# Optimization experiments

Measured on AMD Instinct MI355X. Metric: run time of the kernel, lower is better.

## Reference

```python
import jax, jax.numpy as jnp
import numpy as np

B, D, H, E, K = 8192, 1024, 4096, 8, 2
LOSS_COEF = 0.01
EPS_COMBINE = float(np.finfo(np.float64).eps)  # np.finfo(float).eps used in combine


def setup_inputs() -> dict:
    key = jax.random.key(0)
    ks = jax.random.split(key, 6)
    s_in = 1.0 / np.sqrt(D)
    s_hid = 1.0 / np.sqrt(H)
    return {
        "x": jax.random.normal(ks[0], (B, D), jnp.float32),
        "w_gate": jax.random.uniform(ks[1], (E, D), jnp.float32, -s_in, s_in),
        "fc1_w": jax.random.uniform(ks[2], (E, H, D), jnp.float32, -s_in, s_in),
        "fc1_b": jax.random.uniform(ks[3], (E, H), jnp.float32, -s_in, s_in),
        "fc2_w": jax.random.uniform(ks[4], (E, D, H), jnp.float32, -s_hid, s_hid),
        "fc2_b": jax.random.uniform(ks[5], (E, D), jnp.float32, -s_hid, s_hid),
    }


def _cv_squared(v):
    # torch .var() uses ddof=1
    return jnp.var(v, ddof=1) / (jnp.mean(v) ** 2 + 1e-10)


def _top_k_gating(x, w_gate):
    # clean logits (noisy_gating=False): [B, E]
    logits = x @ w_gate.T
    top_vals, top_idx = jax.lax.top_k(logits, K + 1)  # min(k+1, E)
    topk_vals = top_vals[:, :K]
    topk_idx = top_idx[:, :K]
    topk_gates = jax.nn.softmax(topk_vals, axis=1)
    gates = jnp.zeros((x.shape[0], E), x.dtype)
    gates = gates.at[jnp.arange(x.shape[0])[:, None], topk_idx].set(topk_gates)
    return gates


def _forward(x, w_gate, fc1_w, fc1_b, fc2_w, fc2_b):
    gates = _top_k_gating(x, w_gate)            # [B, E], sparse (k nonzeros/row)
    importance = gates.sum(axis=0)              # [E]
    load = (gates > 0).sum(axis=0).astype(jnp.float32)
    loss = (_cv_squared(importance) + _cv_squared(load)) * LOSS_COEF

    # Dense-equivalent expert compute: tokens with gate==0 contribute 0 to the
    # combine, identical math to SparseDispatcher's gather/scatter.
    h = jnp.einsum('bd,ehd->beh', x, fc1_w) + fc1_b            # [B, E, H]
    h = jax.nn.gelu(h, approximate=False)                      # torch exact gelu
    o = jnp.einsum('beh,edh->bed', h, fc2_w) + fc2_b           # [B, E, D]
    log_p = jax.nn.log_softmax(o, axis=-1)                     # LogSoftmax(dim=1)

    # combine: exp, weight by gates, scatter-add, eps-fill, log
    combined = jnp.einsum('be,bed->bd', gates, jnp.exp(log_p)) # [B, D]
    combined = jnp.where(combined == 0, EPS_COMBINE, combined)
    y = jnp.log(combined)
    return y, loss


def reference(x, w_gate, fc1_w, fc1_b, fc2_w, fc2_b):
    return _forward(x, w_gate, fc1_w, fc1_b, fc2_w, fc2_b)
```

## Files before the change

### kernel.cpp

```cpp
#include <hip/hip_runtime.h>
#include <cstdint>
#include <cmath>

#define BT 8192
#define DD 1024
#define HH 4096
#define EE 8
#define MT2 72

typedef __attribute__((ext_vector_type(8))) short short8;
typedef __attribute__((ext_vector_type(4))) float f32x4;
typedef unsigned short u16;
typedef unsigned int u32;

__device__ __forceinline__ u16 f2bf(float f) {
    u32 u = __float_as_uint(f);
    u += 0x7FFFu + ((u >> 16) & 1u);
    return (u16)(u >> 16);
}

__device__ __forceinline__ void gld_lds16(const void* g, void* l) {
    __builtin_amdgcn_global_load_lds((__attribute__((address_space(1))) void*)g,
                                     (__attribute__((address_space(3))) void*)l,
                                     16, 0, 0);
}

__global__ void cvt_kernel(const float* __restrict__ src, u16* __restrict__ dst, int n8) {
    int i = blockIdx.x * blockDim.x + threadIdx.x;
    if (i >= n8) return;
    size_t base = (size_t)i * 8;
    float4 a = *(const float4*)(src + base);
    float4 b = *(const float4*)(src + base + 4);
    uint4 o;
    o.x = (u32)f2bf(a.x) | ((u32)f2bf(a.y) << 16);
    o.y = (u32)f2bf(a.z) | ((u32)f2bf(a.w) << 16);
    o.z = (u32)f2bf(b.x) | ((u32)f2bf(b.y) << 16);
    o.w = (u32)f2bf(b.z) | ((u32)f2bf(b.w) << 16);
    *(uint4*)(dst + base) = o;
}

__global__ void gating_kernel(const float* __restrict__ x, const float* __restrict__ wg,
                              float* __restrict__ gate_arr, int* __restrict__ list,
                              int* __restrict__ info,
                              int* __restrict__ counts, float* __restrict__ importance) {
    int wave = (blockIdx.x * blockDim.x + threadIdx.x) >> 6;
    int lane = threadIdx.x & 63;
    if (wave >= BT) return;
    const float* xr = x + (size_t)wave * DD;
    double acc[EE];
#pragma unroll
    for (int e = 0; e < EE; ++e) acc[e] = 0.0;
#pragma unroll
    for (int c = 0; c < DD / 256; ++c) {
        const int i = c * 256 + lane * 4;
        float4 xv = *(const float4*)(xr + i);
        double x0 = xv.x, x1 = xv.y, x2 = xv.z, x3 = xv.w;
#pragma unroll
        for (int e = 0; e < EE; ++e) {
            float4 wv = *(const float4*)(wg + e * DD + i);
            acc[e] += x0 * (double)wv.x + x1 * (double)wv.y
                    + x2 * (double)wv.z + x3 * (double)wv.w;
        }
    }
#pragma unroll
    for (int e = 0; e < EE; ++e) {
        double v = acc[e];
        for (int off = 32; off; off >>= 1) v += __shfl_down(v, off, 64);
        acc[e] = v;
    }
    if (lane == 0) {
        int i0 = 0; double v0 = acc[0];
        for (int e = 1; e < EE; ++e) if (acc[e] > v0) { v0 = acc[e]; i0 = e; }
        int i1 = -1; double v1 = -1e300;
        for (int e = 0; e < EE; ++e) { if (e == i0) continue; if (acc[e] > v1) { v1 = acc[e]; i1 = e; } }
        double e1 = exp(v1 - v0);
        double s = 1.0 + e1;
        float g0 = (float)(1.0 / s);
        float g1 = (float)(e1 / s);
        gate_arr[2 * wave]     = g0;
        gate_arr[2 * wave + 1] = g1;
        atomicAdd(&importance[i0], g0);
        atomicAdd(&importance[i1], g1);
        int p0 = atomicAdd(&counts[i0], 1);
        list[i0 * BT + p0] = wave;
        int p1 = atomicAdd(&counts[i1], 1);
        list[i1 * BT + p1] = wave;
        info[2 * wave]     = (i0 << 16) | p0;
        info[2 * wave + 1] = (i1 << 16) | p1;
    }
}

__global__ void loss_kernel(const int* __restrict__ counts, const float* __restrict__ importance,
                            int* __restrict__ offs, float* __restrict__ out_loss,
                            int* __restrict__ tmap, int* __restrict__ ntiles) {
    if (threadIdx.x == 0 && blockIdx.x == 0) {
        double mi = 0, ml = 0;
        int off = 0;
        for (int e = 0; e < EE; e++) {
            offs[e] = off; off += counts[e];
            mi += (double)importance[e]; ml += (double)counts[e];
        }
        mi /= EE; ml /= EE;
        double vi = 0, vl = 0;
        for (int e = 0; e < EE; e++) {
            double di = (double)importance[e] - mi; vi += di * di;
            double dl = (double)counts[e] - ml;     vl += dl * dl;
        }
        vi /= (EE - 1); vl /= (EE - 1);
        double cv_i = vi / (mi * mi + 1e-10);
        double cv_l = vl / (ml * ml + 1e-10);
        *out_loss = (float)((cv_i + cv_l) * 0.01);
        int ntl = 0;
        for (int e = 0; e < EE; e++)
            for (int t = 0; t < counts[e]; t += 256)
                tmap[ntl++] = (e << 20) | t;
        *ntiles = ntl;
    }
}

__global__ void gather_x_kernel(const float* __restrict__ x, const int* __restrict__ list,
                                const int* __restrict__ counts, const int* __restrict__ offs,
                                u16* __restrict__ xg) {
    int r = blockIdx.x;
    int e = 0;
#pragma unroll
    for (int i = 1; i < EE; ++i) if (r >= offs[i]) e = i;
    int m = r - offs[e];
    if (m >= counts[e]) return;
    int token = list[e * BT + m];
    const float* src = x + (size_t)token * DD;
    u16* dst = xg + (size_t)r * DD;
    int i = threadIdx.x * 4;
    float4 a = *(const float4*)(src + i);
    uint2 o;
    o.x = (u32)f2bf(a.x) | ((u32)f2bf(a.y) << 16);
    o.y = (u32)f2bf(a.z) | ((u32)f2bf(a.w) << 16);
    *(uint2*)(dst + i) = o;
}

template <int K, int NT, bool GELU, bool GATHER>
__global__ __launch_bounds__(512) void moe_gemm(const u16* __restrict__ Asrc,
                                                const u16* __restrict__ Bsrc,
                                                const float* __restrict__ bias,
                                                const int* __restrict__ list,
                                                const int* __restrict__ counts,
                                                const int* __restrict__ offs,
                                                const int* __restrict__ tmap,
                                                const int* __restrict__ ntiles,
                                                u16* __restrict__ outB,
                                                float* __restrict__ outF) {
    constexpr int NXT = NT / 256;
    constexpr int nwg = NXT * MT2;
    constexpr int QW = nwg / 8;
    constexpr int ITERS = K / 128;
    const int tid = threadIdx.x;
    const int lane = tid & 63;
    const int wv = tid >> 6;
    const int wqr = wv >> 2;
    const int wqc = wv & 3;
    const int kq = lane >> 4;
    const int rsub = lane & 15;
    const int rq = kq * 4;
    const int ks1 = tid >> 7;
    const int r128 = tid & 127;

    __shared__ u16 Ls[2][2][2][8192];

    const int nw = *ntiles;

#define STAGE_A(db, h, T)                                                   \
    do {                                                                    \
        gld_lds16(aP##h + (T) * 64,      &Ls[db][0][h][tid * 8]);           \
        gld_lds16(aP##h + (T) * 64 + 32, &Ls[db][0][h][(tid + 512) * 8]);   \
    } while (0)
#define STAGE_B(db, h, T)                                                   \
    do {                                                                    \
        gld_lds16(bP##h + (T) * 64,      &Ls[db][1][h][tid * 8]);           \
        gld_lds16(bP##h + (T) * 64 + 32, &Ls[db][1][h][(tid + 512) * 8]);   \
    } while (0)
#define WAIT4 asm volatile("s_waitcnt vmcnt(4)" ::: "memory")
#define WAIT0 asm volatile("s_waitcnt vmcnt(0)" ::: "memory")
#define BAR __builtin_amdgcn_s_barrier()

#define READ_A(db, mh)                                                        \
    do {                                                                      \
        _Pragma("unroll") for (int kk = 0; kk < 2; kk++)                      \
        _Pragma("unroll") for (int mi = 0; mi < 4; mi++)                      \
            afr[mi][kk] = *(const short8*)&Ls[db][0][mh]                      \
                [((kk * 4 + kq) * 128 + wqr * 64 + mi * 16 + rsub) * 8];      \
    } while (0)
#define READ_B(nh, db)                                                        \
    do {                                                                      \
        _Pragma("unroll") for (int kk = 0; kk < 2; kk++)                      \
        _Pragma("unroll") for (int ni = 0; ni < 2; ni++)                      \
            bfr[nh][ni][kk] = *(const short8*)&Ls[db][1][nh]                  \
                [((kk * 4 + kq) * 128 + wqc * 32 + ni * 16 + rsub) * 8];      \
    } while (0)
#define MFMAQ(mh, nh)                                                         \
    do {                                                                      \
        __builtin_amdgcn_s_setprio(1);                                        \
        _Pragma("unroll") for (int mi = 0; mi < 4; mi++)                      \
        _Pragma("unroll") for (int ni = 0; ni < 2; ni++)                      \
        _Pragma("unroll") for (int kk = 0; kk < 2; kk++)                      \
            acc[mh][nh][mi][ni] = __builtin_amdgcn_mfma_f32_16x16x32_bf16(    \
                afr[mi][kk], bfr[nh][ni][kk], acc[mh][nh][mi][ni], 0, 0, 0);  \
        __builtin_amdgcn_s_setprio(0);                                        \
    } while (0)

#pragma unroll 1
    for (int raw = blockIdx.x; raw < nwg; raw += 256) {
        const int wg = (raw & 7) * QW + (raw >> 3);
        const int nt = wg / MT2;
        const int mt = wg - nt * MT2;
        if (mt >= nw) continue;
        const int ent = tmap[mt];
        const int e = ent >> 20;
        const int mbase = ent & 0xFFFFF;
        const int mmax = counts[e] - mbase;
        const int rowbase = offs[e] + mbase;
        const int nbase = nt * 256;

        size_t arow0, arow1;
        if constexpr (GATHER) {
            arow0 = (size_t)list[e * BT + mbase + min(r128, mmax - 1)];
            arow1 = (size_t)list[e * BT + mbase + min(128 + r128, mmax - 1)];
        } else {
            arow0 = (size_t)(rowbase + min(r128, mmax - 1));
            arow1 = (size_t)(rowbase + min(128 + r128, mmax - 1));
        }
        const u16* aP0 = Asrc + arow0 * (size_t)K + ks1 * 8;
        const u16* aP1 = Asrc + arow1 * (size_t)K + ks1 * 8;
        const u16* bP0 = Bsrc + ((size_t)e * NT + nbase + r128) * (size_t)K + ks1 * 8;
        const u16* bP1 = bP0 + (size_t)128 * K;

        f32x4 acc[2][2][4][2] = {};
        short8 afr[4][2];
        short8 bfr[2][2][2];

        STAGE_A(0, 0, 0); STAGE_B(0, 0, 0); STAGE_A(0, 1, 0); STAGE_B(0, 1, 0);
        STAGE_A(1, 0, 1); STAGE_B(1, 0, 1);
        WAIT4;
        BAR;

#pragma unroll 1
        for (int it = 0; it < ITERS - 1; ++it) {
            const int t = 2 * it;
            READ_A(0, 0); READ_B(0, 0); STAGE_A(1, 1, t + 1); MFMAQ(0, 0); BAR;
            READ_B(1, 0); STAGE_B(1, 1, t + 1); MFMAQ(0, 1); BAR;
            READ_A(0, 1); STAGE_A(0, 0, t + 2); MFMAQ(1, 0); BAR;
            STAGE_B(0, 0, t + 2); MFMAQ(1, 1); WAIT4; BAR;
            READ_A(1, 0); READ_B(0, 1); STAGE_A(0, 1, t + 2); MFMAQ(0, 0); BAR;
            READ_B(1, 1); STAGE_B(0, 1, t + 2); MFMAQ(0, 1); BAR;
            READ_A(1, 1); STAGE_A(1, 0, t + 3); MFMAQ(1, 0); BAR;
            STAGE_B(1, 0, t + 3); MFMAQ(1, 1); WAIT4; BAR;
        }
        {
            const int t = 2 * (ITERS - 1);
            READ_A(0, 0); READ_B(0, 0); STAGE_A(1, 1, t + 1); MFMAQ(0, 0); BAR;
            READ_B(1, 0); STAGE_B(1, 1, t + 1); MFMAQ(0, 1); BAR;
            READ_A(0, 1); MFMAQ(1, 0); BAR;
            MFMAQ(1, 1); WAIT0; BAR;
            READ_A(1, 0); READ_B(0, 1); MFMAQ(0, 0); BAR;
            READ_B(1, 1); MFMAQ(0, 1); BAR;
            READ_A(1, 1); MFMAQ(1, 0); BAR;
            MFMAQ(1, 1); BAR;
        }

        float bvals[2][2];
#pragma unroll
        for (int nh = 0; nh < 2; nh++)
#pragma unroll
            for (int ni = 0; ni < 2; ni++)
                bvals[nh][ni] = bias[(size_t)e * NT + nbase + nh * 128 + wqc * 32 + ni * 16 + rsub];
#pragma unroll
        for (int mh = 0; mh < 2; mh++) {
#pragma unroll
            for (int mi = 0; mi < 4; mi++) {
#pragma unroll
                for (int r = 0; r < 4; r++) {
                    int m = mh * 128 + wqr * 64 + mi * 16 + rq + r;
                    if (m < mmax) {
                        size_t ro = (size_t)(rowbase + m);
#pragma unroll
                        for (int nh = 0; nh < 2; nh++) {
#pragma unroll
                            for (int ni = 0; ni < 2; ni++) {
                                int n = nbase + nh * 128 + wqc * 32 + ni * 16 + rsub;
                                float v = acc[mh][nh][mi][ni][r] + bvals[nh][ni];
                                if constexpr (GELU) {
                                    v = 0.5f * v * (1.0f + erff(v * 0.7071067811865476f));
                                    outB[ro * NT + n] = f2bf(v);
                                } else {
                                    outF[ro * NT + n] = v;
                                }
                            }
                        }
                    }
                }
            }
        }
        WAIT0;
    }
#undef READ_A
#undef READ_B
#undef MFMAQ
#undef STAGE_A
#undef STAGE_B
#undef WAIT4
#undef WAIT0
#undef BAR
}

__global__ void combine_kernel(const float* __restrict__ o, const float* __restrict__ gates,
                               const int* __restrict__ info, const int* __restrict__ offs,
                               float* __restrict__ y) {
    const int b = blockIdx.x;
    const int tid = threadIdx.x;
    const int lane = tid & 63, wv = tid >> 6;
    const int inf0 = info[2 * b], inf1 = info[2 * b + 1];
    const int r0i = offs[inf0 >> 16] + (inf0 & 0xffff);
    const int r1i = offs[inf1 >> 16] + (inf1 & 0xffff);
    const float* r0 = o + (size_t)r0i * DD;
    const float* r1 = o + (size_t)r1i * DD;
    float v0[4], v1[4];
#pragma unroll
    for (int j = 0; j < 4; j++) { v0[j] = r0[tid + 256 * j]; v1[j] = r1[tid + 256 * j]; }
    float m0 = fmaxf(fmaxf(v0[0], v0[1]), fmaxf(v0[2], v0[3]));
    float m1 = fmaxf(fmaxf(v1[0], v1[1]), fmaxf(v1[2], v1[3]));
#pragma unroll
    for (int off = 32; off; off >>= 1) {
        m0 = fmaxf(m0, __shfl_xor(m0, off, 64));
        m1 = fmaxf(m1, __shfl_xor(m1, off, 64));
    }
    __shared__ float sred[2][4];
    if (lane == 0) { sred[0][wv] = m0; sred[1][wv] = m1; }
    __syncthreads();
    m0 = fmaxf(fmaxf(sred[0][0], sred[0][1]), fmaxf(sred[0][2], sred[0][3]));
    m1 = fmaxf(fmaxf(sred[1][0], sred[1][1]), fmaxf(sred[1][2], sred[1][3]));
    float p0[4], p1[4], s0 = 0.f, s1 = 0.f;
#pragma unroll
    for (int j = 0; j < 4; j++) {
        p0[j] = expf(v0[j] - m0); s0 += p0[j];
        p1[j] = expf(v1[j] - m1); s1 += p1[j];
    }
#pragma unroll
    for (int off = 32; off; off >>= 1) {
        s0 += __shfl_xor(s0, off, 64);
        s1 += __shfl_xor(s1, off, 64);
    }
    __shared__ float sred2[2][4];
    if (lane == 0) { sred2[0][wv] = s0; sred2[1][wv] = s1; }
    __syncthreads();
    s0 = sred2[0][0] + sred2[0][1] + sred2[0][2] + sred2[0][3];
    s1 = sred2[1][0] + sred2[1][1] + sred2[1][2] + sred2[1][3];
    const float c0 = gates[2 * b] / s0;
    const float c1 = gates[2 * b + 1] / s1;
#pragma unroll
    for (int j = 0; j < 4; j++) {
        float c = p0[j] * c0 + p1[j] * c1;
        if (c == 0.f) c = 2.2204460492503131e-16f;
        y[(size_t)b * DD + tid + 256 * j] = logf(c);
    }
}

extern "C" void kernel_launch(void* const* d_in, const int* in_sizes, int n_in,
                              void* d_out, int out_size, void* d_ws, size_t ws_size,
                              hipStream_t stream) {
    const float* x     = (const float*)d_in[0];
    const float* wgate = (const float*)d_in[1];
    const float* fc1w  = (const float*)d_in[2];
    const float* fc1b  = (const float*)d_in[3];
    const float* fc2w  = (const float*)d_in[4];
    const float* fc2b  = (const float*)d_in[5];
    float* out = (float*)d_out;

    char* ws = (char*)d_ws;
    const size_t MB = 1024 * 1024;
    const bool big = ws_size >= 289 * MB;
    u16* w1b = (u16*)(ws);
    float* o = (float*)(ws);
    u16* w2b = (u16*)(ws + 64 * MB);
    u16* xb  = (u16*)(ws + 128 * MB);
    u16* h   = (u16*)(ws + (big ? 128 : 144) * MB);
    u16* xg  = (u16*)(ws + 256 * MB);
    char* meta = ws + (big ? 288 : 272) * MB;
    int* counts       = (int*)meta;
    int* offs         = (int*)(meta + 32);
    float* importance = (float*)(meta + 64);
    int* ntiles       = (int*)(meta + 96);
    float* gate_arr   = (float*)(meta + 128);
    int* info         = (int*)(meta + 128 + 65536);
    int* list         = (int*)(meta + 128 + 131072);
    int* tmap         = (int*)(meta + 512 * 1024);

    hipMemsetAsync(meta, 0, 96, stream);
    cvt_kernel<<<(EE * HH * DD / 8 + 255) / 256, 256, 0, stream>>>(fc1w, w1b, EE * HH * DD / 8);
    cvt_kernel<<<(EE * DD * HH / 8 + 255) / 256, 256, 0, stream>>>(fc2w, w2b, EE * DD * HH / 8);
    gating_kernel<<<BT / 4, 256, 0, stream>>>(x, wgate, gate_arr, list, info, counts, importance);
    loss_kernel<<<1, 64, 0, stream>>>(counts, importance, offs, out + (size_t)BT * DD, tmap, ntiles);

    if (big) {
        gather_x_kernel<<<2 * BT, 256, 0, stream>>>(x, list, counts, offs, xg);
        moe_gemm<DD, HH, true, false><<<256, 512, 0, stream>>>(
            xg, w1b, fc1b, nullptr, counts, offs, tmap, ntiles, h, nullptr);
    } else {
        cvt_kernel<<<(BT * DD / 8 + 255) / 256, 256, 0, stream>>>(x, xb, BT * DD / 8);
        moe_gemm<DD, HH, true, true><<<256, 512, 0, stream>>>(
            xb, w1b, fc1b, list, counts, offs, tmap, ntiles, h, nullptr);
    }
    moe_gemm<HH, DD, false, false><<<256, 512, 0, stream>>>(
        h, w2b, fc2b, nullptr, counts, offs, tmap, ntiles, nullptr, o);
    combine_kernel<<<BT, 256, 0, stream>>>(o, gate_arr, info, offs, out);
}
```

Baseline: 1.174 ms.

## Shrink MoE GEMM output tile to 256x128 with a single B buffer

Changes the expert GEMM workgroup tile from 256x256 to 256x128 (M x N). The 8 waves are rearranged as 4x2, each computing 64x64 instead of 128x64. LDS staging now holds two A halves and one B buffer per stage, and the pipeline is restructured into four MFMA phases per iteration with adjusted vmcnt waits. This doubles the number of N tiles, which gives more workgroups for the persistent loop and cuts LDS use. The cost is lower arithmetic intensity: A is re-read twice as often from global memory, and there is more barrier overhead per MFMA.

```diff
diff --git a/kernel.cpp b/kernel.cpp
--- a/kernel.cpp
+++ b/kernel.cpp
@@ -149,57 +149,59 @@
                                                 const int* __restrict__ ntiles,
                                                 u16* __restrict__ outB,
                                                 float* __restrict__ outF) {
-    constexpr int NXT = NT / 256;
+    constexpr int NXT = NT / 128;
     constexpr int nwg = NXT * MT2;
     constexpr int QW = nwg / 8;
     constexpr int ITERS = K / 128;
     const int tid = threadIdx.x;
     const int lane = tid & 63;
     const int wv = tid >> 6;
-    const int wqr = wv >> 2;
-    const int wqc = wv & 3;
+    const int wqm = wv >> 1;
+    const int wqn = wv & 1;
     const int kq = lane >> 4;
     const int rsub = lane & 15;
     const int rq = kq * 4;
     const int ks1 = tid >> 7;
     const int r128 = tid & 127;
 
-    __shared__ u16 Ls[2][2][2][8192];
+    __shared__ u16 Ls[2][3][8192];
 
     const int nw = *ntiles;
 
 #define STAGE_A(db, h, T)                                                   \
     do {                                                                    \
-        gld_lds16(aP##h + (T) * 64,      &Ls[db][0][h][tid * 8]);           \
-        gld_lds16(aP##h + (T) * 64 + 32, &Ls[db][0][h][(tid + 512) * 8]);   \
+        gld_lds16(aP##h + (T) * 64,      &Ls[db][h][tid * 8]);              \
+        gld_lds16(aP##h + (T) * 64 + 32, &Ls[db][h][(tid + 512) * 8]);      \
     } while (0)
-#define STAGE_B(db, h, T)                                                   \
+#define STAGE_B(db, T)                                                      \
     do {                                                                    \
-        gld_lds16(bP##h + (T) * 64,      &Ls[db][1][h][tid * 8]);           \
-        gld_lds16(bP##h + (T) * 64 + 32, &Ls[db][1][h][(tid + 512) * 8]);   \
+        gld_lds16(bP + (T) * 64,      &Ls[db][2][tid * 8]);                 \
+        gld_lds16(bP + (T) * 64 + 32, &Ls[db][2][(tid + 512) * 8]);         \
     } while (0)
-#define WAIT4 asm volatile("s_waitcnt vmcnt(4)" ::: "memory")
+#define WAIT2 asm volatile("s_waitcnt vmcnt(2)" ::: "memory")
 #define WAIT0 asm volatile("s_waitcnt vmcnt(0)" ::: "memory")
 #define BAR __builtin_amdgcn_s_barrier()
 
 #define READ_A(db, mh)                                                        \
     do {                                                                      \
         _Pragma("unroll") for (int kk = 0; kk < 2; kk++)                      \
-        _Pragma("unroll") for (int mi = 0; mi < 4; mi++)                      \
-            afr[mi][kk] = *(const short8*)&Ls[db][0][mh]                      \
-                [((kk * 4 + kq) * 128 + wqr * 64 + mi * 16 + rsub) * 8];      \
+        _Pragma("unroll") for (int mi = 0; mi < 2; mi++)                      \
+            afr[mi][kk] = *(const short8*)&Ls[db][mh]                         \
+                [((kk * 4 + kq) * 128 + wqm * 32 + mi * 16 + rsub) * 8];      \
     } while (0)
-#define READ_B(nh, db)                                                        \
+#define READ_B(db)                                                            \
     do {                                                                      \
         _Pragma("unroll") for (int kk = 0; kk < 2; kk++)                      \
+        _Pragma("unroll") for (int nh = 0; nh < 2; nh++)                      \
         _Pragma("unroll") for (int ni = 0; ni < 2; ni++)                      \
-            bfr[nh][ni][kk] = *(const short8*)&Ls[db][1][nh]                  \
-                [((kk * 4 + kq) * 128 + wqc * 32 + ni * 16 + rsub) * 8];      \
+            bfr[nh][ni][kk] = *(const short8*)&Ls[db][2]                      \
+                [((kk * 4 + kq) * 128 + nh * 64 + wqn * 32 + ni * 16 + rsub) * 8]; \
     } while (0)
-#define MFMAQ(mh, nh)                                                         \
+#define MFMAH(mh)                                                             \
     do {                                                                      \
         __builtin_amdgcn_s_setprio(1);                                        \
-        _Pragma("unroll") for (int mi = 0; mi < 4; mi++)                      \
+        _Pragma("unroll") for (int nh = 0; nh < 2; nh++)                      \
+        _Pragma("unroll") for (int mi = 0; mi < 2; mi++)                      \
         _Pragma("unroll") for (int ni = 0; ni < 2; ni++)                      \
         _Pragma("unroll") for (int kk = 0; kk < 2; kk++)                      \
             acc[mh][nh][mi][ni] = __builtin_amdgcn_mfma_f32_16x16x32_bf16(    \
@@ -218,7 +220,7 @@
         const int mbase = ent & 0xFFFFF;
         const int mmax = counts[e] - mbase;
         const int rowbase = offs[e] + mbase;
-        const int nbase = nt * 256;
+        const int nbase = nt * 128;
 
         size_t arow0, arow1;
         if constexpr (GATHER) {
@@ -230,40 +232,44 @@
         }
         const u16* aP0 = Asrc + arow0 * (size_t)K + ks1 * 8;
         const u16* aP1 = Asrc + arow1 * (size_t)K + ks1 * 8;
-        const u16* bP0 = Bsrc + ((size_t)e * NT + nbase + r128) * (size_t)K + ks1 * 8;
-        const u16* bP1 = bP0 + (size_t)128 * K;
-
-        f32x4 acc[2][2][4][2] = {};
-        short8 afr[4][2];
+        const u16* bP  = Bsrc + ((size_t)e * NT + nbase + r128) * (size_t)K + ks1 * 8;
+
+        f32x4 acc[2][2][2][2] = {};
+        short8 afr[2][2];
         short8 bfr[2][2][2];
 
-        STAGE_A(0, 0, 0); STAGE_B(0, 0, 0); STAGE_A(0, 1, 0); STAGE_B(0, 1, 0);
-        STAGE_A(1, 0, 1); STAGE_B(1, 0, 1);
-        WAIT4;
+        STAGE_A(0, 0, 0); STAGE_A(0, 1, 0); STAGE_B(0, 0);
+        STAGE_A(1, 0, 1);
+        WAIT2;
         BAR;
 
 #pragma unroll 1
         for (int it = 0; it < ITERS - 1; ++it) {
             const int t = 2 * it;
-            READ_A(0, 0); READ_B(0, 0); STAGE_A(1, 1, t + 1); MFMAQ(0, 0); BAR;
-            READ_B(1, 0); STAGE_B(1, 1, t + 1); MFMAQ(0, 1); BAR;
-            READ_A(0, 1); STAGE_A(0, 0, t + 2); MFMAQ(1, 0); BAR;
-            STAGE_B(0, 0, t + 2); MFMAQ(1, 1); WAIT4; BAR;
-            READ_A(1, 0); READ_B(0, 1); STAGE_A(0, 1, t + 2); MFMAQ(0, 0); BAR;
-            READ_B(1, 1); STAGE_B(0, 1, t + 2); MFMAQ(0, 1); BAR;
-            READ_A(1, 1); STAGE_A(1, 0, t + 3); MFMAQ(1, 0); BAR;
-            STAGE_B(1, 0, t + 3); MFMAQ(1, 1); WAIT4; BAR;
+            READ_A(0, 0); READ_B(0);
+            STAGE_A(1, 1, t + 1); STAGE_B(1, t + 1);
+            MFMAH(0); BAR;
+            READ_A(0, 1);
+            STAGE_A(0, 0, t + 2);
+            MFMAH(1); WAIT2; BAR;
+            READ_A(1, 0); READ_B(1);
+            STAGE_A(0, 1, t + 2); STAGE_B(0, t + 2);
+            MFMAH(0); BAR;
+            READ_A(1, 1);
+            STAGE_A(1, 0, t + 3);
+            MFMAH(1); WAIT2; BAR;
         }
         {
             const int t = 2 * (ITERS - 1);
-            READ_A(0, 0); READ_B(0, 0); STAGE_A(1, 1, t + 1); MFMAQ(0, 0); BAR;
-            READ_B(1, 0); STAGE_B(1, 1, t + 1); MFMAQ(0, 1); BAR;
-            READ_A(0, 1); MFMAQ(1, 0); BAR;
-            MFMAQ(1, 1); WAIT0; BAR;
-            READ_A(1, 0); READ_B(0, 1); MFMAQ(0, 0); BAR;
-            READ_B(1, 1); MFMAQ(0, 1); BAR;
-            READ_A(1, 1); MFMAQ(1, 0); BAR;
-            MFMAQ(1, 1); BAR;
+            READ_A(0, 0); READ_B(0);
+            STAGE_A(1, 1, t + 1); STAGE_B(1, t + 1);
+            MFMAH(0); BAR;
+            READ_A(0, 1);
+            MFMAH(1); WAIT0; BAR;
+            READ_A(1, 0); READ_B(1);
+            MFMAH(0); BAR;
+            READ_A(1, 1);
+            MFMAH(1); BAR;
         }
 
         float bvals[2][2];
@@ -271,21 +277,21 @@
         for (int nh = 0; nh < 2; nh++)
 #pragma unroll
             for (int ni = 0; ni < 2; ni++)
-                bvals[nh][ni] = bias[(size_t)e * NT + nbase + nh * 128 + wqc * 32 + ni * 16 + rsub];
+                bvals[nh][ni] = bias[(size_t)e * NT + nbase + nh * 64 + wqn * 32 + ni * 16 + rsub];
 #pragma unroll
         for (int mh = 0; mh < 2; mh++) {
 #pragma unroll
-            for (int mi = 0; mi < 4; mi++) {
+            for (int mi = 0; mi < 2; mi++) {
 #pragma unroll
                 for (int r = 0; r < 4; r++) {
-                    int m = mh * 128 + wqr * 64 + mi * 16 + rq + r;
+                    int m = mh * 128 + wqm * 32 + mi * 16 + rq + r;
                     if (m < mmax) {
                         size_t ro = (size_t)(rowbase + m);
 #pragma unroll
                         for (int nh = 0; nh < 2; nh++) {
 #pragma unroll
                             for (int ni = 0; ni < 2; ni++) {
-                                int n = nbase + nh * 128 + wqc * 32 + ni * 16 + rsub;
+                                int n = nbase + nh * 64 + wqn * 32 + ni * 16 + rsub;
                                 float v = acc[mh][nh][mi][ni][r] + bvals[nh][ni];
                                 if constexpr (GELU) {
                                     v = 0.5f * v * (1.0f + erff(v * 0.7071067811865476f));
@@ -303,10 +309,10 @@
     }
 #undef READ_A
 #undef READ_B
-#undef MFMAQ
+#undef MFMAH
 #undef STAGE_A
 #undef STAGE_B
-#undef WAIT4
+#undef WAIT2
 #undef WAIT0
 #undef BAR
 }
```

After: 1.251 ms. +6.6%, slower.
